# Optimization experiments

Hardware: AMD Instinct MI355X
Metric: run time of the kernel (lower is better)

The kernel has to match this reference:

```python
import jax, jax.numpy as jnp
import numpy as np

B = 100          # batch_size -> dist matrix is [2B, 2B]
G = 2            # pairs
REG = 0.1
H = W = 256
EPS = 1e-08


def computemask(b, g):
    # Faithful numpy port of the torch computemask (pure python, constants).
    Mask, labels = [], []
    mtxsize = 2 * b
    for j in range(mtxsize):
        i = j
        x = [i - i % g - i // b * b,
             i + 1 - i % g - i // b * b,
             i - i % g - i // b * b + b,
             i + 1 - i % g - i // b * b + b]
        x.remove(j)
        for xi in x:
            xx = x.copy()
            indexs = list(range(mtxsize))
            indexs.remove(j)
            xx.remove(xi)
            for r in xx:
                indexs.remove(r)
            labels.append(indexs.index(xi))
            Mask.append(indexs)
    return np.asarray(Mask, np.int32), np.asarray(labels, np.int32)


def setup_inputs() -> dict:
    key = jax.random.key(0)
    x = jax.random.normal(key, (2 * B, 1, H, W), dtype=jnp.float32)
    m, l = computemask(B, G)              # [6B, 2B-3], [6B]
    return {"x": x, "masks": jnp.asarray(m), "labels": jnp.asarray(l)}


def _euclidean_distance_matrix(x):
    xf = x.reshape(x.shape[0], -1)                      # [N, H*W]
    dot = xf @ xf.T                                     # [N, N] Gram GEMM
    sq = jnp.diagonal(dot)
    d = sq[None, :] - 2.0 * dot + sq[:, None]
    d = jnp.maximum(d, 0.0)
    mask = (d == 0.0).astype(x.dtype)
    d = jnp.sqrt(d + mask * EPS) * (1.0 - mask)
    return d


def _calc_psd(xs):
    dft = jnp.fft.fft2(xs)                              # [N, H, W] complex
    avgpsd = jnp.mean((dft * jnp.conj(dft)).real, axis=0)  # [H, W]
    return jnp.mean(jnp.log(avgpsd)) - jnp.log(jnp.mean(avgpsd))


def reference(x, masks, labels):
    xs = jnp.squeeze(x)                                 # [2B, H, W]
    dist = _euclidean_distance_matrix(xs)               # [2B, 2B]
    # create_pairs: logits[m] = dist[m // 3][masks[m]]  -> [6B, 2B-3]
    rows = jnp.arange(masks.shape[0]) // 3
    logits = dist[rows[:, None], masks]
    logp = jax.nn.log_softmax(logits, axis=-1)
    ce = -jnp.mean(logp[jnp.arange(labels.shape[0]), labels])
    return ce - REG * _calc_psd(xs)
```

## Files before the change

### kernel.cpp

```cpp
#include <hip/hip_runtime.h>
#include <hip/hip_bf16.h>
#include <math.h>


#define NIMG 200
#define NROW 256
#define NCOL 256
#define NPIX 65536
#define TSTR 132
#define ISTR 264
#define XSTR 273
#define NCH  25
#define GNK  64
#define GKC  1024

typedef float2 c2;
typedef short bf16x8 __attribute__((ext_vector_type(8)));
typedef unsigned short u16x8 __attribute__((ext_vector_type(8)));
typedef float f32x4  __attribute__((ext_vector_type(4)));

__device__ __forceinline__ unsigned short f2b(float f) {
    union { float f; unsigned int u; } c; c.f = f;
    unsigned int r = (c.u + 0x7FFFu + ((c.u >> 16) & 1u)) >> 16;
    return (unsigned short)r;
}
__device__ __forceinline__ float b2f(unsigned short b) {
    union { unsigned int u; float f; } c; c.u = ((unsigned int)b) << 16;
    return c.f;
}

__device__ __forceinline__ c2 cmul(c2 a, c2 b) {
    return make_float2(a.x*b.x - a.y*b.y, a.x*b.y + a.y*b.x);
}
__device__ __forceinline__ c2 cadd(c2 a, c2 b){ return make_float2(a.x+b.x, a.y+b.y); }
__device__ __forceinline__ c2 csub(c2 a, c2 b){ return make_float2(a.x-b.x, a.y-b.y); }
__device__ __forceinline__ c2 mulmi(c2 a){ return make_float2(a.y, -a.x); }

__device__ __forceinline__ void fft4(c2& a, c2& b, c2& c, c2& d) {
    c2 t0 = cadd(a,c), t1 = csub(a,c), t2 = cadd(b,d), t3 = csub(b,d);
    a = cadd(t0,t2);
    c = csub(t0,t2);
    c2 mt3 = mulmi(t3);
    b = cadd(t1, mt3);
    d = csub(t1, mt3);
}

__device__ __forceinline__ void fft16(c2 x[16]) {
    #pragma unroll
    for (int j=0;j<4;j++) fft4(x[j], x[4+j], x[8+j], x[12+j]);
    const c2 W1 = make_float2( 0.9238795325112867f,-0.3826834323650898f);
    const c2 W2 = make_float2( 0.7071067811865476f,-0.7071067811865476f);
    const c2 W3 = make_float2( 0.3826834323650898f,-0.9238795325112867f);
    const c2 W6 = make_float2(-0.7071067811865476f,-0.7071067811865476f);
    const c2 W9 = make_float2(-0.9238795325112867f, 0.3826834323650898f);
    x[5]=cmul(x[5],W1);   x[6]=cmul(x[6],W2);   x[7]=cmul(x[7],W3);
    x[9]=cmul(x[9],W2);   x[10]=mulmi(x[10]);   x[11]=cmul(x[11],W6);
    x[13]=cmul(x[13],W3); x[14]=cmul(x[14],W6); x[15]=cmul(x[15],W9);
    #pragma unroll
    for (int k1=0;k1<4;k1++) fft4(x[4*k1], x[4*k1+1], x[4*k1+2], x[4*k1+3]);
}
#define R4(q) ((((q)&3)<<2)|((q)>>2))

__global__ __launch_bounds__(512) void k_gemm(const unsigned short* __restrict__ Xb,
                                              float* __restrict__ Pg) {
    __shared__ unsigned short As[128*64];
    __shared__ unsigned short Bs[128*64];
    int p  = blockIdx.x;
    int kc = blockIdx.y;
    int ti = p >> 1, tj = (p + 1) >> 1;
    bool diag = (ti == tj);
    int i0 = ti << 7, j0 = tj << 7;
    int tid = threadIdx.x;
    int wid = tid >> 6, lane = tid & 63;
    int wr = wid >> 2, wc = wid & 3;

    f32x4 acc[4][2];
    #pragma unroll
    for (int a=0;a<4;a++)
        #pragma unroll
        for (int b=0;b<2;b++) acc[a][b] = (f32x4){0.f,0.f,0.f,0.f};

    int srow = tid >> 2, g0 = (tid & 3) * 2;
    int gia = i0 + srow; if (gia > 199) gia = 199;
    int gjb = j0 + srow; if (gjb > 199) gjb = 199;
    const u16x8* Ap = (const u16x8*)(Xb + (size_t)gia*NPIX + kc*GKC);
    const u16x8* Bp = (const u16x8*)(Xb + (size_t)gjb*NPIX + kc*GKC);
    int e0 = (srow*128 + g0*16) ^ ((srow & 7) << 4);
    int e1 = (srow*128 + (g0+1)*16) ^ ((srow & 7) << 4);

    int swz = (lane & 7) << 3;
    int acol0 = (lane >> 4) << 3;

    u16x8 ca0 = Ap[g0], ca1 = Ap[g0+1];
    u16x8 cb0, cb1;
    if (!diag) { cb0 = Bp[g0]; cb1 = Bp[g0+1]; }

    for (int st = 0; st < GKC/64; ++st) {
        __syncthreads();
        *(u16x8*)((char*)As + e0) = ca0;
        *(u16x8*)((char*)As + e1) = ca1;
        if (!diag) {
            *(u16x8*)((char*)Bs + e0) = cb0;
            *(u16x8*)((char*)Bs + e1) = cb1;
        }
        if (st < GKC/64 - 1) {
            ca0 = Ap[(st+1)*8 + g0]; ca1 = Ap[(st+1)*8 + g0+1];
            if (!diag) { cb0 = Bp[(st+1)*8 + g0]; cb1 = Bp[(st+1)*8 + g0+1]; }
        }
        __syncthreads();
        const unsigned short* Bb = diag ? As : Bs;
        #pragma unroll
        for (int ks=0; ks<2; ++ks) {
            int col = (ks*32 + acol0) ^ swz;
            bf16x8 af[4], bfv[2];
            #pragma unroll
            for (int mf=0; mf<4; ++mf) {
                int r = wr*64 + mf*16 + (lane & 15);
                af[mf] = *(const bf16x8*)(&As[r*64 + col]);
            }
            #pragma unroll
            for (int nf=0; nf<2; ++nf) {
                int r = wc*32 + nf*16 + (lane & 15);
                bfv[nf] = *(const bf16x8*)(&Bb[r*64 + col]);
            }
            #pragma unroll
            for (int mf=0; mf<4; ++mf)
                #pragma unroll
                for (int nf=0; nf<2; ++nf)
                    acc[mf][nf] = __builtin_amdgcn_mfma_f32_16x16x32_bf16(af[mf], bfv[nf], acc[mf][nf], 0, 0, 0);
        }
    }
    float* P = Pg + ((size_t)p*GNK + kc)*16384;
    #pragma unroll
    for (int mf=0; mf<4; ++mf) {
        int m0 = wr*64 + mf*16 + ((lane >> 4) << 2);
        #pragma unroll
        for (int nf=0; nf<2; ++nf) {
            int n = wc*32 + nf*16 + (lane & 15);
            #pragma unroll
            for (int r2=0; r2<4; ++r2)
                P[(size_t)(m0+r2)*128 + n] = acc[mf][nf][r2];
        }
    }
}

__global__ __launch_bounds__(256) void k_gredu(const float* __restrict__ Pg,
                                               float* __restrict__ dotm) {
    int idx = blockIdx.x*256 + threadIdx.x;
    if (idx >= 200*200) return;
    int i = idx / 200, j = idx - i*200;
    int ti = i >> 7, tj = j >> 7;
    int p, li, lj;
    if (ti <= tj) { p = ti + tj; li = i - (ti << 7); lj = j - (tj << 7); }
    else          { p = 1;       li = j;             lj = i - 128; }
    const float* base = Pg + (size_t)p*GNK*16384 + (size_t)li*128 + lj;
    float s = 0.f;
    #pragma unroll 8
    for (int kc=0; kc<GNK; ++kc) s += base[(size_t)kc*16384];
    dotm[(size_t)i*200 + j] = s;
}

__global__ __launch_bounds__(256) void k_rowfft(const float* __restrict__ x,
                                                ushort2* __restrict__ T,
                                                unsigned short* __restrict__ Xb) {
    __shared__ __align__(16) char ldsraw[16*XSTR*4];
    float*   inpF = (float*)ldsraw;
    ushort2* tb   = (ushort2*)ldsraw;
    int tid = threadIdx.x;
    int img = blockIdx.y;
    int rg  = blockIdx.x;
    int g = tid >> 4, t = tid & 15;
    int row = rg*16 + g;

    const float4* xr = (const float4*)(x + (size_t)img*NPIX + (size_t)row*NCOL + t*16);
    float4 v0 = xr[0], v1 = xr[1], v2 = xr[2], v3 = xr[3];
    u16x8 h0, h1;
    h0[0]=f2b(v0.x); h0[1]=f2b(v0.y); h0[2]=f2b(v0.z); h0[3]=f2b(v0.w);
    h0[4]=f2b(v1.x); h0[5]=f2b(v1.y); h0[6]=f2b(v1.z); h0[7]=f2b(v1.w);
    h1[0]=f2b(v2.x); h1[1]=f2b(v2.y); h1[2]=f2b(v2.z); h1[3]=f2b(v2.w);
    h1[4]=f2b(v3.x); h1[5]=f2b(v3.y); h1[6]=f2b(v3.z); h1[7]=f2b(v3.w);
    u16x8* Xo = (u16x8*)(Xb + (size_t)img*NPIX + (size_t)row*NCOL + t*16);
    Xo[0] = h0; Xo[1] = h1;
    float* ip = inpF + g*ISTR + t*16;
    *(float4*)(ip)    = v0;
    *(float4*)(ip+4)  = v1;
    *(float4*)(ip+8)  = v2;
    *(float4*)(ip+12) = v3;
    __syncthreads();

    c2 y[16];
    #pragma unroll
    for (int n1=0;n1<16;n1++) y[n1] = make_float2(inpF[g*ISTR + 16*n1 + t], 0.f);
    fft16(y);
    {
        float sv, cv;
        sincosf(-0.024543692606170259f * (float)t, &sv, &cv);
        c2 Wb = make_float2(cv, sv);
        c2 cur = Wb;
        #pragma unroll
        for (int r=1;r<16;r++) { y[R4(r)] = cmul(y[R4(r)], cur); cur = cmul(cur, Wb); }
    }
    __syncthreads();
    #pragma unroll
    for (int r=0;r<16;r++) {
        c2 v = y[R4(r)];
        tb[g*XSTR + t*17 + r] = make_ushort2(f2b(v.x), f2b(v.y));
    }
    __syncthreads();

    c2 w[16];
    #pragma unroll
    for (int n2=0;n2<16;n2++) {
        ushort2 u = tb[g*XSTR + n2*17 + t];
        w[n2] = make_float2(b2f(u.x), b2f(u.y));
    }
    fft16(w);
    ushort2* To = T + ((size_t)img*NROW + row)*TSTR;
    #pragma unroll
    for (int q=0;q<8;q++) {
        c2 v = w[R4(q)];
        To[q*16 + t] = make_ushort2(f2b(v.x), f2b(v.y));
    }
    if (t == 0) { c2 v = w[R4(8)]; To[128] = make_ushort2(f2b(v.x), f2b(v.y)); }
}

__global__ __launch_bounds__(256) void k_colfft(const ushort2* __restrict__ T,
                                                float* __restrict__ Ppart) {
    __shared__ ushort2 sb[16][XSTR];
    int tid = threadIdx.x;
    int c0 = blockIdx.x * 16;
    int ic = blockIdx.y;
    int g = tid >> 4, t = tid & 15;
    int cc = tid & 15, rb = tid >> 4;
    int cl = c0 + cc; if (cl > 128) cl = 128;
    c2 Wb;
    {
        float sv, cv;
        sincosf(-0.024543692606170259f * (float)t, &sv, &cv);
        Wb = make_float2(cv, sv);
    }
    float pacc[16];
    #pragma unroll
    for (int q=0;q<16;q++) pacc[q] = 0.f;

    for (int li=0; li<8; ++li) {
        int img = ic*8 + li;
        __syncthreads();
        const ushort2* Tb = T + (size_t)img*NROW*TSTR;
        #pragma unroll
        for (int j=0;j<16;j++) {
            int r = rb*16 + j;
            sb[cc][r] = Tb[(size_t)r*TSTR + cl];
        }
        __syncthreads();
        c2 y[16];
        #pragma unroll
        for (int n1=0;n1<16;n1++) {
            ushort2 u = sb[g][16*n1 + t];
            y[n1] = make_float2(b2f(u.x), b2f(u.y));
        }
        fft16(y);
        {
            c2 cur = Wb;
            #pragma unroll
            for (int r=1;r<16;r++) { y[R4(r)] = cmul(y[R4(r)], cur); cur = cmul(cur, Wb); }
        }
        __syncthreads();
        #pragma unroll
        for (int r=0;r<16;r++) {
            c2 v = y[R4(r)];
            sb[g][t*17 + r] = make_ushort2(f2b(v.x), f2b(v.y));
        }
        __syncthreads();
        c2 w[16];
        #pragma unroll
        for (int n2=0;n2<16;n2++) {
            ushort2 u = sb[g][n2*17 + t];
            w[n2] = make_float2(b2f(u.x), b2f(u.y));
        }
        fft16(w);
        #pragma unroll
        for (int q=0;q<16;q++) { c2 v = w[R4(q)]; pacc[q] += v.x*v.x + v.y*v.y; }
    }
    int c = c0 + g;
    if (c <= 128) {
        float* PP = Ppart + ((size_t)ic*132 + c)*256;
        #pragma unroll
        for (int q=0;q<16;q++) PP[q*16 + t] = pacc[q];
    }
}

__global__ __launch_bounds__(64) void k_distce(const float* __restrict__ dotm,
                                               const int* __restrict__ masks,
                                               const int* __restrict__ labels,
                                               float* __restrict__ cep) {
    int m = blockIdx.x;
    int lane = threadIdx.x;
    int i = m / 3;
    float sqi = dotm[(size_t)i*200 + i];
    int lbl = labels[m];
    float lg[4];
    float vmax = -1e30f, lsel = 0.f;
    #pragma unroll
    for (int k=0;k<4;k++) {
        int c = lane + 64*k;
        float v = -1e30f;
        if (c < 197) {
            int j = masks[(size_t)m*197 + c];
            float d = sqi + dotm[(size_t)j*200 + j] - 2.f*dotm[(size_t)i*200 + j];
            d = fmaxf(d, 0.f);
            v = (d == 0.f) ? 0.f : sqrtf(d);
            if (c == lbl) lsel = v;
        }
        lg[k] = v;
        vmax = fmaxf(vmax, v);
    }
    #pragma unroll
    for (int off=32; off>=1; off>>=1) vmax = fmaxf(vmax, __shfl_xor(vmax, off));
    float se = 0.f;
    #pragma unroll
    for (int k=0;k<4;k++) if (lg[k] > -1e29f) se += expf(lg[k] - vmax);
    #pragma unroll
    for (int off=32; off>=1; off>>=1) { se += __shfl_xor(se, off); lsel += __shfl_xor(lsel, off); }
    if (lane == 0) cep[m] = lsel - (vmax + logf(se));
}

__global__ __launch_bounds__(256) void k_reduce(const float* __restrict__ Ppart,
                                                float2* __restrict__ Pred) {
    int c = blockIdx.x, tid = threadIdx.x;
    float s = 0.f;
    for (int ic=0; ic<NCH; ++ic) s += Ppart[((size_t)ic*132 + c)*256 + tid];
    float v = s * (1.0f/200.0f);
    float w = (c == 0 || c == 128) ? 1.f : 2.f;
    float sl = w * logf(v);
    float ss = w * v;
    __shared__ float r2[2][4];
    int wv = tid>>6, ln = tid&63;
    #pragma unroll
    for (int off=32; off>=1; off>>=1) {
        sl += __shfl_xor(sl, off);
        ss += __shfl_xor(ss, off);
    }
    if (ln == 0) { r2[0][wv] = sl; r2[1][wv] = ss; }
    __syncthreads();
    if (tid == 0)
        Pred[c] = make_float2(r2[0][0]+r2[0][1]+r2[0][2]+r2[0][3],
                              r2[1][0]+r2[1][1]+r2[1][2]+r2[1][3]);
}

__global__ __launch_bounds__(256) void k_final(const float2* __restrict__ Pred,
                                               const float* __restrict__ cep,
                                               float* __restrict__ out) {
    int tid = threadIdx.x;
    float sl = 0.f, ss = 0.f, sce = 0.f;
    if (tid < 129) { float2 p = Pred[tid]; sl = p.x; ss = p.y; }
    for (int m = tid; m < 600; m += 256) sce += cep[m];
    __shared__ float r3[3][4];
    int wv = tid>>6, ln = tid&63;
    #pragma unroll
    for (int off=32; off>=1; off>>=1) {
        sl  += __shfl_xor(sl, off);
        ss  += __shfl_xor(ss, off);
        sce += __shfl_xor(sce, off);
    }
    if (ln == 0) { r3[0][wv]=sl; r3[1][wv]=ss; r3[2][wv]=sce; }
    __syncthreads();
    if (tid == 0) {
        float SL = r3[0][0]+r3[0][1]+r3[0][2]+r3[0][3];
        float SS = r3[1][0]+r3[1][1]+r3[1][2]+r3[1][3];
        float CE = r3[2][0]+r3[2][1]+r3[2][2]+r3[2][3];
        float ce  = -CE / 600.f;
        float psd = SL * (1.f/65536.f) - logf(SS * (1.f/65536.f));
        out[0] = ce - 0.1f * psd;
    }
}

extern "C" void kernel_launch(void* const* d_in, const int* in_sizes, int n_in,
                              void* d_out, int out_size, void* d_ws, size_t ws_size,
                              hipStream_t stream) {
    const float* x      = (const float*)d_in[0];
    const int*   masks  = (const int*)d_in[1];
    const int*   labels = (const int*)d_in[2];
    float* out = (float*)d_out;
    char* ws = (char*)d_ws;

    const size_t OFF_DOT = 0;
    const size_t OFF_CE  = 160256;
    const size_t OFF_PR  = 162688;
    const size_t OFF_PP  = 163840;
    const size_t OFF_T   = 3543040;
    const size_t OFF_XB  = 30576640;
    const size_t OFF_PG  = 56791040;
    const size_t NEED    = 69373952;
    if (ws_size < NEED) return;

    float*          dotm = (float*)(ws + OFF_DOT);
    float*          cep  = (float*)(ws + OFF_CE);
    float2*         Pr   = (float2*)(ws + OFF_PR);
    float*          Pp   = (float*)(ws + OFF_PP);
    ushort2*        T    = (ushort2*)(ws + OFF_T);
    unsigned short* Xb   = (unsigned short*)(ws + OFF_XB);
    float*          Pg   = (float*)(ws + OFF_PG);

    k_rowfft<<<dim3(16,200), dim3(256), 0, stream>>>(x, T, Xb);
    k_gemm  <<<dim3(3, GNK), dim3(512), 0, stream>>>(Xb, Pg);
    k_gredu <<<dim3(157),    dim3(256), 0, stream>>>(Pg, dotm);
    k_colfft<<<dim3(9,25),   dim3(256), 0, stream>>>(T, Pp);
    k_distce<<<dim3(600),    dim3(64),  0, stream>>>(dotm, masks, labels, cep);
    k_reduce<<<dim3(129),    dim3(256), 0, stream>>>(Pp, Pr);
    k_final <<<dim3(1),      dim3(256), 0, stream>>>(Pr, cep, out);
}
```

Before: 84.29 us.

## Double-buffer GEMM LDS tiles, double split-K, and rotate row-FFT LDS writes

The GEMM now double-buffers its LDS tiles, prefetching two stages ahead, so each stage needs one barrier instead of two. Split-K goes from 64 to 128 chunks of 512, giving more blocks but more partial sums for k_gredu to read and a larger workspace. k_gredu sums with four independent accumulators to shorten the dependency chain. In k_rowfft, the float4 stores to LDS are rotated per thread group to cut bank conflicts, and the strided reads are remapped to match.

```diff
diff --git a/kernel.cpp b/kernel.cpp
--- a/kernel.cpp
+++ b/kernel.cpp
@@ -11,8 +11,9 @@
 #define ISTR 264
 #define XSTR 273
 #define NCH  25
-#define GNK  64
-#define GKC  1024
+#define GNK  128
+#define GKC  512
+#define NST  8
 
 typedef float2 c2;
 typedef short bf16x8 __attribute__((ext_vector_type(8)));
@@ -63,8 +64,8 @@
 
 __global__ __launch_bounds__(512) void k_gemm(const unsigned short* __restrict__ Xb,
                                               float* __restrict__ Pg) {
-    __shared__ unsigned short As[128*64];
-    __shared__ unsigned short Bs[128*64];
+    __shared__ unsigned short As[2*8192];
+    __shared__ unsigned short Bs[2*8192];
     int p  = blockIdx.x;
     int kc = blockIdx.y;
     int ti = p >> 1, tj = (p + 1) >> 1;
@@ -94,21 +95,34 @@
     u16x8 ca0 = Ap[g0], ca1 = Ap[g0+1];
     u16x8 cb0, cb1;
     if (!diag) { cb0 = Bp[g0]; cb1 = Bp[g0+1]; }
-
-    for (int st = 0; st < GKC/64; ++st) {
-        __syncthreads();
-        *(u16x8*)((char*)As + e0) = ca0;
-        *(u16x8*)((char*)As + e1) = ca1;
-        if (!diag) {
-            *(u16x8*)((char*)Bs + e0) = cb0;
-            *(u16x8*)((char*)Bs + e1) = cb1;
-        }
-        if (st < GKC/64 - 1) {
-            ca0 = Ap[(st+1)*8 + g0]; ca1 = Ap[(st+1)*8 + g0+1];
-            if (!diag) { cb0 = Bp[(st+1)*8 + g0]; cb1 = Bp[(st+1)*8 + g0+1]; }
-        }
-        __syncthreads();
-        const unsigned short* Bb = diag ? As : Bs;
+    *(u16x8*)((char*)As + e0) = ca0;
+    *(u16x8*)((char*)As + e1) = ca1;
+    if (!diag) {
+        *(u16x8*)((char*)Bs + e0) = cb0;
+        *(u16x8*)((char*)Bs + e1) = cb1;
+    }
+    ca0 = Ap[8 + g0]; ca1 = Ap[8 + g0+1];
+    if (!diag) { cb0 = Bp[8 + g0]; cb1 = Bp[8 + g0+1]; }
+    __syncthreads();
+
+    for (int st = 0; st < NST; ++st) {
+        int cur = st & 1;
+        if (st + 1 < NST) {
+            char* Aw = (char*)As + ((cur^1) << 14);
+            *(u16x8*)(Aw + e0) = ca0;
+            *(u16x8*)(Aw + e1) = ca1;
+            if (!diag) {
+                char* Bw = (char*)Bs + ((cur^1) << 14);
+                *(u16x8*)(Bw + e0) = cb0;
+                *(u16x8*)(Bw + e1) = cb1;
+            }
+        }
+        if (st + 2 < NST) {
+            ca0 = Ap[(st+2)*8 + g0]; ca1 = Ap[(st+2)*8 + g0+1];
+            if (!diag) { cb0 = Bp[(st+2)*8 + g0]; cb1 = Bp[(st+2)*8 + g0+1]; }
+        }
+        const unsigned short* Ab = As + cur*8192;
+        const unsigned short* Bb = diag ? Ab : (Bs + cur*8192);
         #pragma unroll
         for (int ks=0; ks<2; ++ks) {
             int col = (ks*32 + acol0) ^ swz;
@@ -116,7 +130,7 @@
             #pragma unroll
             for (int mf=0; mf<4; ++mf) {
                 int r = wr*64 + mf*16 + (lane & 15);
-                af[mf] = *(const bf16x8*)(&As[r*64 + col]);
+                af[mf] = *(const bf16x8*)(&Ab[r*64 + col]);
             }
             #pragma unroll
             for (int nf=0; nf<2; ++nf) {
@@ -129,6 +143,7 @@
                 for (int nf=0; nf<2; ++nf)
                     acc[mf][nf] = __builtin_amdgcn_mfma_f32_16x16x32_bf16(af[mf], bfv[nf], acc[mf][nf], 0, 0, 0);
         }
+        __syncthreads();
     }
     float* P = Pg + ((size_t)p*GNK + kc)*16384;
     #pragma unroll
@@ -154,10 +169,15 @@
     if (ti <= tj) { p = ti + tj; li = i - (ti << 7); lj = j - (tj << 7); }
     else          { p = 1;       li = j;             lj = i - 128; }
     const float* base = Pg + (size_t)p*GNK*16384 + (size_t)li*128 + lj;
-    float s = 0.f;
+    float s0=0.f, s1=0.f, s2=0.f, s3=0.f;
     #pragma unroll 8
-    for (int kc=0; kc<GNK; ++kc) s += base[(size_t)kc*16384];
-    dotm[(size_t)i*200 + j] = s;
+    for (int kc=0; kc<GNK; kc+=4) {
+        s0 += base[(size_t)(kc  )*16384];
+        s1 += base[(size_t)(kc+1)*16384];
+        s2 += base[(size_t)(kc+2)*16384];
+        s3 += base[(size_t)(kc+3)*16384];
+    }
+    dotm[(size_t)i*200 + j] = (s0+s1) + (s2+s3);
 }
 
 __global__ __launch_bounds__(256) void k_rowfft(const float* __restrict__ x,
@@ -181,16 +201,22 @@
     h1[4]=f2b(v3.x); h1[5]=f2b(v3.y); h1[6]=f2b(v3.z); h1[7]=f2b(v3.w);
     u16x8* Xo = (u16x8*)(Xb + (size_t)img*NPIX + (size_t)row*NCOL + t*16);
     Xo[0] = h0; Xo[1] = h1;
-    float* ip = inpF + g*ISTR + t*16;
-    *(float4*)(ip)    = v0;
-    *(float4*)(ip+4)  = v1;
-    *(float4*)(ip+8)  = v2;
-    *(float4*)(ip+12) = v3;
+    {
+        float* ip = inpF + g*ISTR + t*16;
+        float4 vv[4] = {v0, v1, v2, v3};
+        int rot = t >> 2;
+        #pragma unroll
+        for (int k=0;k<4;k++)
+            *(float4*)(ip + (((k + rot) & 3) << 2)) = vv[k];
+    }
     __syncthreads();
 
     c2 y[16];
     #pragma unroll
-    for (int n1=0;n1<16;n1++) y[n1] = make_float2(inpF[g*ISTR + 16*n1 + t], 0.f);
+    for (int n1=0;n1<16;n1++) {
+        int phys = 16*n1 + ((((t>>2) + (n1>>2)) & 3) << 2) + (t & 3);
+        y[n1] = make_float2(inpF[g*ISTR + phys], 0.f);
+    }
     fft16(y);
     {
         float sv, cv;
@@ -391,7 +417,7 @@
     const size_t OFF_T   = 3543040;
     const size_t OFF_XB  = 30576640;
     const size_t OFF_PG  = 56791040;
-    const size_t NEED    = 69373952;
+    const size_t NEED    = 81956864;
     if (ws_size < NEED) return;
 
     float*          dotm = (float*)(ws + OFF_DOT);
```

After: 97.57 us. 1.16x slower.
